# Kernel optimization log

Hardware: AMD Instinct MI355X
Metric: run time of the kernel (lower is better)

Reference implementation:

```python
import jax, jax.numpy as jnp
import numpy as np

B, S, H, E, V = 64, 1024, 1024, 1024, 50257


def setup_inputs() -> dict:
    key = jax.random.key(0)
    ks = jax.random.split(key, 12)
    x = jax.random.randint(ks[0], (B, 1), 0, V, dtype=jnp.int64)
    h = jax.random.normal(ks[1], (B, H), dtype=jnp.float32)
    c = jax.random.normal(ks[2], (B, H), dtype=jnp.float32)
    encoder_output = jax.random.normal(ks[3], (B, S, H), dtype=jnp.float32)
    length = jax.random.randint(ks[4], (B,), 1, S + 1, dtype=jnp.int32)
    length = length.at[0].set(S)  # mask width is length[0]; must equal S
    scale = 0.02
    emb = jax.random.normal(ks[5], (V, E), dtype=jnp.float32) * scale
    W_ih = jax.random.normal(ks[6], (4 * H, E), dtype=jnp.float32) * scale
    b_ih = jnp.zeros((4 * H,), dtype=jnp.float32)
    W_hh = jax.random.normal(ks[7], (4 * H, H), dtype=jnp.float32) * scale
    b_hh = jnp.zeros((4 * H,), dtype=jnp.float32)
    W_bilin = jax.random.normal(ks[8], (H, H), dtype=jnp.float32) * scale
    W_out = jax.random.normal(ks[9], (V, 2 * H), dtype=jnp.float32) * scale
    b_out = jnp.zeros((V,), dtype=jnp.float32)
    return {"x": x, "h": h, "c": c, "encoder_output": encoder_output,
            "length": length, "emb": emb, "W_ih": W_ih, "b_ih": b_ih,
            "W_hh": W_hh, "b_hh": b_hh, "W_bilin": W_bilin,
            "W_out": W_out, "b_out": b_out}


def reference(x, h, c, encoder_output, length, emb, W_ih, b_ih, W_hh, b_hh,
              W_bilin, W_out, b_out):
    # embedding + squeeze(1); dropout is identity in eval mode
    xe = emb[x[:, 0]]  # [B, E]
    # LSTMCell: gates in PyTorch order i, f, g, o
    gates = xe @ W_ih.T + b_ih + h @ W_hh.T + b_hh  # [B, 4H]
    i_g, f_g, g_g, o_g = jnp.split(gates, 4, axis=-1)
    i_g = jax.nn.sigmoid(i_g)
    f_g = jax.nn.sigmoid(f_g)
    g_g = jnp.tanh(g_g)
    o_g = jax.nn.sigmoid(o_g)
    c_new = f_g * c + i_g * g_g
    h_new = o_g * jnp.tanh(c_new)  # [B, H]
    # bilinear attention energy: (h W) . enc
    energy = jnp.einsum('bh,hk,bsk->bs', h_new, W_bilin, encoder_output)
    # mask multiplies energy BEFORE softmax (faithful to original code)
    mask = (jnp.arange(S)[None, :] < length[:, None]).astype(energy.dtype)
    attn = jax.nn.softmax(energy * mask, axis=-1)  # [B, S]
    context = jnp.einsum('bs,bsh->bh', attn, encoder_output)  # [B, H]
    output = jnp.concatenate([context, h_new], axis=1) @ W_out.T + b_out  # [B, V]
    return output, h_new, c_new
```

## Files before the change

kernel.cpp:

```cpp
#include <hip/hip_runtime.h>
#include <math.h>

constexpr int NB = 64;
constexpr int NS = 1024;
constexpr int NH = 1024;
constexpr int NE = 1024;
constexpr int NV = 50257;
constexpr int NK2 = 2048;

typedef __bf16 bf16_8 __attribute__((ext_vector_type(8)));
typedef float  f32x4  __attribute__((ext_vector_type(4)));

__device__ inline f32x4 ntload4(const float* p) {
  return __builtin_nontemporal_load((const f32x4*)p);
}

__global__ __launch_bounds__(256) void k_cvtAg(const int* __restrict__ x,
    const float* __restrict__ h, const float* __restrict__ emb,
    __bf16* __restrict__ Ag) {
  int t = blockIdx.x * 256 + threadIdx.x;
  int b = t >> 11, k = t & 2047;
  float v = (k < NE) ? emb[(size_t)x[b] * NE + k] : h[b * NH + (k - NE)];
  Ag[t] = (__bf16)v;
}

__global__ __launch_bounds__(256) void k_gates_mfma(const __bf16* __restrict__ Ag,
    const float* __restrict__ Wih, const float* __restrict__ bih,
    const float* __restrict__ Whh, const float* __restrict__ bhh,
    float* __restrict__ gates) {
  __shared__ f32x4 red[4][4][64];
  int lane = threadIdx.x & 63;
  int wave = threadIdx.x >> 6;
  int col  = lane & 15;
  int grp  = lane >> 4;
  int j    = blockIdx.x * 16 + col;

  const float* Wsel = (wave < 2) ? Wih : Whh;
  const float*  wp  = Wsel + (size_t)j * 1024 + (wave & 1) * 512 + grp * 8;
  const __bf16* ap  = Ag + wave * 512 + grp * 8;

  f32x4 acc[4] = {};
#pragma unroll 4
  for (int ks = 0; ks < 16; ++ks) {
    int kb = ks * 32;
    f32x4 b0 = ntload4(wp + kb);
    f32x4 b1 = ntload4(wp + kb + 4);
    bf16_8 bf;
    bf[0] = (__bf16)b0[0]; bf[1] = (__bf16)b0[1];
    bf[2] = (__bf16)b0[2]; bf[3] = (__bf16)b0[3];
    bf[4] = (__bf16)b1[0]; bf[5] = (__bf16)b1[1];
    bf[6] = (__bf16)b1[2]; bf[7] = (__bf16)b1[3];
#pragma unroll
    for (int m = 0; m < 4; ++m) {
      bf16_8 a = *(const bf16_8*)(ap + (m * 16 + col) * NK2 + kb);
      acc[m] = __builtin_amdgcn_mfma_f32_16x16x32_bf16(a, bf, acc[m], 0, 0, 0);
    }
  }
#pragma unroll
  for (int m = 0; m < 4; ++m) red[wave][m][lane] = acc[m];
  __syncthreads();
  f32x4 s = red[0][wave][lane];
#pragma unroll
  for (int wv = 1; wv < 4; ++wv) s += red[wv][wave][lane];
  float bias = bih[j] + bhh[j];
  int b = wave * 16 + grp * 4;
#pragma unroll
  for (int r = 0; r < 4; ++r)
    gates[(b + r) * 4096 + j] = s[r] + bias;
}

__global__ __launch_bounds__(256) void k_lstm(const float* __restrict__ gates,
    const float* __restrict__ c, float* __restrict__ hc_out,
    __bf16* __restrict__ A_bf) {
  int t = blockIdx.x * 256 + threadIdx.x;
  int b = t >> 10, hh = t & 1023;
  float ig = gates[b * 4096 + hh];
  float fg = gates[b * 4096 + 1024 + hh];
  float gg = gates[b * 4096 + 2048 + hh];
  float og = gates[b * 4096 + 3072 + hh];
  float i_ = 1.f / (1.f + expf(-ig));
  float f_ = 1.f / (1.f + expf(-fg));
  float g_ = tanhf(gg);
  float o_ = 1.f / (1.f + expf(-og));
  float cn = f_ * c[t] + i_ * g_;
  float hn = o_ * tanhf(cn);
  hc_out[t] = hn;
  hc_out[NB * NH + t] = cn;
  A_bf[b * NK2 + 1024 + hh] = (__bf16)hn;
}

__global__ __launch_bounds__(256) void k_bilin(const float* __restrict__ hnew,
    const float* __restrict__ Wb, float* __restrict__ t_out) {
  int b = blockIdx.x >> 2;
  int k = ((blockIdx.x & 3) << 8) + threadIdx.x;
  const float* hb = hnew + b * NH;
  float acc = 0.f;
#pragma unroll 8
  for (int hh = 0; hh < NH; ++hh)
    acc += hb[hh] * Wb[hh * NH + k];
  t_out[b * NH + k] = acc;
}

__global__ __launch_bounds__(256) void k_attn(const float* __restrict__ t_in,
    const float* __restrict__ enc, const int* __restrict__ length,
    float* __restrict__ ctxp, float* __restrict__ ml) {
  int b     = blockIdx.x >> 4;
  int strip = ((blockIdx.x & 15) << 2) + (threadIdx.x >> 6);
  int lane  = threadIdx.x & 63;
  int len   = length[b];
  int s0    = strip * 16;

  const float* tp = t_in + b * NH;
  f32x4 tv[4];
#pragma unroll
  for (int i = 0; i < 4; ++i) tv[i] = *(const f32x4*)(tp + (i * 64 + lane) * 4);

  const float* ep = enc + ((size_t)b * NS + s0) * NH;

  float m_run = -1e30f, l_run = 0.f;
  f32x4 acc[4] = {};

#pragma unroll 2
  for (int r = 0; r < 16; ++r) {
    f32x4 e[4];
#pragma unroll
    for (int i = 0; i < 4; ++i) e[i] = ntload4(ep + (r * 256 + i * 64 + lane) * 4);
    float d = 0.f;
#pragma unroll
    for (int i = 0; i < 4; ++i)
      d += tv[i][0] * e[i][0] + tv[i][1] * e[i][1] + tv[i][2] * e[i][2] + tv[i][3] * e[i][3];
#pragma unroll
    for (int off = 32; off; off >>= 1) d += __shfl_xor(d, off);
    float v = (s0 + r < len) ? d : 0.f;
    float m_new = fmaxf(m_run, v);
    float f = expf(m_run - m_new);
    float w = expf(v - m_new);
    l_run = l_run * f + w;
#pragma unroll
    for (int i = 0; i < 4; ++i)
      acc[i] = acc[i] * f + w * e[i];
    m_run = m_new;
  }

  int idx = b * 64 + strip;
  float* P = ctxp + (size_t)idx * 1024;
#pragma unroll
  for (int i = 0; i < 4; ++i)
    *(f32x4*)(P + (i * 64 + lane) * 4) = acc[i];
  if (lane == 0) {
    ml[idx * 2]     = m_run;
    ml[idx * 2 + 1] = l_run;
  }
}

__global__ __launch_bounds__(256) void k_attn_combine(const float* __restrict__ ctxp,
    const float* __restrict__ ml, __bf16* __restrict__ A_bf) {
  int b = blockIdx.x;
  int tid = threadIdx.x;
  float M = -1e30f;
#pragma unroll
  for (int c = 0; c < 64; ++c) M = fmaxf(M, ml[(b * 64 + c) * 2]);
  float Z = 0.f;
  f32x4 num = {0.f, 0.f, 0.f, 0.f};
#pragma unroll 4
  for (int c = 0; c < 64; ++c) {
    float e = expf(ml[(b * 64 + c) * 2] - M);
    Z += e * ml[(b * 64 + c) * 2 + 1];
    f32x4 p = *(const f32x4*)(ctxp + ((size_t)(b * 64 + c)) * 1024 + tid * 4);
    num += e * p;
  }
  float inv = 1.f / Z;
  __bf16* dst = A_bf + b * NK2 + tid * 4;
#pragma unroll
  for (int i = 0; i < 4; ++i) dst[i] = (__bf16)(num[i] * inv);
}

__global__ __launch_bounds__(64) void k_out_mfma(const __bf16* __restrict__ A,
    const float* __restrict__ Wout, const float* __restrict__ bout,
    float* __restrict__ out) {
  int lane = threadIdx.x;
  int col  = lane & 15;
  int grp  = lane >> 4;
  int vb   = blockIdx.x * 32;
  int va   = vb + col;
  int vc   = vb + 16 + col;
  int vaC  = va < NV ? va : NV - 1;
  int vcC  = vc < NV ? vc : NV - 1;

  const float*  wpA = Wout + (size_t)vaC * NK2 + grp * 8;
  const float*  wpB = Wout + (size_t)vcC * NK2 + grp * 8;
  const __bf16* ap  = A + grp * 8;

  f32x4 acc[4][2] = {};

#pragma unroll 2
  for (int ks = 0; ks < 64; ++ks) {
    int kb = ks * 32;
    f32x4 a0 = ntload4(wpA + kb);
    f32x4 a1 = ntload4(wpA + kb + 4);
    f32x4 c0 = ntload4(wpB + kb);
    f32x4 c1 = ntload4(wpB + kb + 4);
    bf16_8 bfA, bfB;
    bfA[0] = (__bf16)a0[0]; bfA[1] = (__bf16)a0[1];
    bfA[2] = (__bf16)a0[2]; bfA[3] = (__bf16)a0[3];
    bfA[4] = (__bf16)a1[0]; bfA[5] = (__bf16)a1[1];
    bfA[6] = (__bf16)a1[2]; bfA[7] = (__bf16)a1[3];
    bfB[0] = (__bf16)c0[0]; bfB[1] = (__bf16)c0[1];
    bfB[2] = (__bf16)c0[2]; bfB[3] = (__bf16)c0[3];
    bfB[4] = (__bf16)c1[0]; bfB[5] = (__bf16)c1[1];
    bfB[6] = (__bf16)c1[2]; bfB[7] = (__bf16)c1[3];
#pragma unroll
    for (int m = 0; m < 4; ++m) {
      bf16_8 a = *(const bf16_8*)(ap + (size_t)(m * 16 + col) * NK2 + kb);
      acc[m][0] = __builtin_amdgcn_mfma_f32_16x16x32_bf16(a, bfA, acc[m][0], 0, 0, 0);
      acc[m][1] = __builtin_amdgcn_mfma_f32_16x16x32_bf16(a, bfB, acc[m][1], 0, 0, 0);
    }
  }

#pragma unroll
  for (int n = 0; n < 2; ++n) {
    int vrow = vb + n * 16 + col;
    if (vrow < NV) {
      float bb = bout[vrow];
      int mrow = grp * 4;
#pragma unroll
      for (int m = 0; m < 4; ++m)
#pragma unroll
        for (int r = 0; r < 4; ++r)
          out[(size_t)(m * 16 + mrow + r) * NV + vrow] = acc[m][n][r] + bb;
    }
  }
}

extern "C" void kernel_launch(void* const* d_in, const int* in_sizes, int n_in,
                              void* d_out, int out_size, void* d_ws, size_t ws_size,
                              hipStream_t stream) {
  const int*   x      = (const int*)d_in[0];
  const float* h      = (const float*)d_in[1];
  const float* c      = (const float*)d_in[2];
  const float* enc    = (const float*)d_in[3];
  const int*   length = (const int*)d_in[4];
  const float* emb    = (const float*)d_in[5];
  const float* Wih    = (const float*)d_in[6];
  const float* bih    = (const float*)d_in[7];
  const float* Whh    = (const float*)d_in[8];
  const float* bhh    = (const float*)d_in[9];
  const float* Wb     = (const float*)d_in[10];
  const float* Wout   = (const float*)d_in[11];
  const float* bout   = (const float*)d_in[12];

  float* out = (float*)d_out;
  float* hn  = out + (size_t)NB * NV;

  float* ws      = (float*)d_ws;
  float* gates   = ws;
  float* t_ws    = gates + NB * 4 * NH;
  float* ctxp    = t_ws + NB * NH;
  float* ml      = ctxp + 64 * (size_t)NB * 1024;
  __bf16* A_bf   = (__bf16*)(ml + NB * 128);
  __bf16* Ag_bf  = A_bf + NB * NK2;

  k_cvtAg<<<NB * NK2 / 256, 256, 0, stream>>>(x, h, emb, Ag_bf);
  k_gates_mfma<<<4096 / 16, 256, 0, stream>>>(Ag_bf, Wih, bih, Whh, bhh, gates);
  k_lstm<<<NB * NH / 256, 256, 0, stream>>>(gates, c, hn, A_bf);
  k_bilin<<<NB * 4, 256, 0, stream>>>(hn, Wb, t_ws);
  k_attn<<<NB * 16, 256, 0, stream>>>(t_ws, enc, length, ctxp, ml);
  k_attn_combine<<<NB, 256, 0, stream>>>(ctxp, ml, A_bf);
  k_out_mfma<<<(NV + 31) / 32, 64, 0, stream>>>(A_bf, Wout, bout, out);
}
```

Baseline: 269.7 us.

## Split output GEMM over K and overlap the h-half with attention

The output projection is split into two K halves. The half that multiplies h_new (the upper 1024 columns of W_out) is computed as extra blocks inside the attention kernel, so its W_out streaming runs concurrently with the encoder streaming. The final kernel then handles only the context half and adds the stored partial sums and the bias. The cost is a 64xV fp32 partial buffer that must be written and read back, and the attention kernel now competes with the GEMM blocks for memory bandwidth.

```diff
diff --git a/kernel.cpp b/kernel.cpp
--- a/kernel.cpp
+++ b/kernel.cpp
@@ -101,12 +101,71 @@
   t_out[b * NH + k] = acc;
 }
 
-__global__ __launch_bounds__(256) void k_attn(const float* __restrict__ t_in,
+constexpr int NOUT1 = (NV + 127) / 128;
+
+__global__ __launch_bounds__(256) void k_attn_out1(const float* __restrict__ t_in,
     const float* __restrict__ enc, const int* __restrict__ length,
-    float* __restrict__ ctxp, float* __restrict__ ml) {
-  int b     = blockIdx.x >> 4;
-  int strip = ((blockIdx.x & 15) << 2) + (threadIdx.x >> 6);
-  int lane  = threadIdx.x & 63;
+    const __bf16* __restrict__ A, const float* __restrict__ Wout,
+    float* __restrict__ ctxp, float* __restrict__ ml, float* __restrict__ part) {
+  int tid  = threadIdx.x;
+  int lane = tid & 63;
+
+  if (blockIdx.x < NOUT1) {
+    int wave = tid >> 6;
+    int col  = lane & 15;
+    int grp  = lane >> 4;
+    int vb   = blockIdx.x * 128 + wave * 32;
+    int va   = vb + col;
+    int vc   = vb + 16 + col;
+    int vaC  = va < NV ? va : NV - 1;
+    int vcC  = vc < NV ? vc : NV - 1;
+
+    const float*  wpA = Wout + (size_t)vaC * NK2 + 1024 + grp * 8;
+    const float*  wpB = Wout + (size_t)vcC * NK2 + 1024 + grp * 8;
+    const __bf16* ap  = A + 1024 + grp * 8;
+
+    f32x4 acc[4][2] = {};
+#pragma unroll 2
+    for (int ks = 0; ks < 32; ++ks) {
+      int kb = ks * 32;
+      f32x4 a0 = ntload4(wpA + kb);
+      f32x4 a1 = ntload4(wpA + kb + 4);
+      f32x4 c0 = ntload4(wpB + kb);
+      f32x4 c1 = ntload4(wpB + kb + 4);
+      bf16_8 bfA, bfB;
+      bfA[0] = (__bf16)a0[0]; bfA[1] = (__bf16)a0[1];
+      bfA[2] = (__bf16)a0[2]; bfA[3] = (__bf16)a0[3];
+      bfA[4] = (__bf16)a1[0]; bfA[5] = (__bf16)a1[1];
+      bfA[6] = (__bf16)a1[2]; bfA[7] = (__bf16)a1[3];
+      bfB[0] = (__bf16)c0[0]; bfB[1] = (__bf16)c0[1];
+      bfB[2] = (__bf16)c0[2]; bfB[3] = (__bf16)c0[3];
+      bfB[4] = (__bf16)c1[0]; bfB[5] = (__bf16)c1[1];
+      bfB[6] = (__bf16)c1[2]; bfB[7] = (__bf16)c1[3];
+#pragma unroll
+      for (int m = 0; m < 4; ++m) {
+        bf16_8 a = *(const bf16_8*)(ap + (size_t)(m * 16 + col) * NK2 + kb);
+        acc[m][0] = __builtin_amdgcn_mfma_f32_16x16x32_bf16(a, bfA, acc[m][0], 0, 0, 0);
+        acc[m][1] = __builtin_amdgcn_mfma_f32_16x16x32_bf16(a, bfB, acc[m][1], 0, 0, 0);
+      }
+    }
+#pragma unroll
+    for (int n = 0; n < 2; ++n) {
+      int vrow = vb + n * 16 + col;
+      if (vrow < NV) {
+        int mrow = grp * 4;
+#pragma unroll
+        for (int m = 0; m < 4; ++m)
+#pragma unroll
+          for (int r = 0; r < 4; ++r)
+            part[(size_t)(m * 16 + mrow + r) * NV + vrow] = acc[m][n][r];
+      }
+    }
+    return;
+  }
+
+  int bid   = blockIdx.x - NOUT1;
+  int b     = bid >> 4;
+  int strip = ((bid & 15) << 2) + (tid >> 6);
   int len   = length[b];
   int s0    = strip * 16;
 
@@ -175,9 +234,9 @@
   for (int i = 0; i < 4; ++i) dst[i] = (__bf16)(num[i] * inv);
 }
 
-__global__ __launch_bounds__(64) void k_out_mfma(const __bf16* __restrict__ A,
+__global__ __launch_bounds__(64) void k_out0(const __bf16* __restrict__ A,
     const float* __restrict__ Wout, const float* __restrict__ bout,
-    float* __restrict__ out) {
+    const float* __restrict__ part, float* __restrict__ out) {
   int lane = threadIdx.x;
   int col  = lane & 15;
   int grp  = lane >> 4;
@@ -194,7 +253,7 @@
   f32x4 acc[4][2] = {};
 
 #pragma unroll 2
-  for (int ks = 0; ks < 64; ++ks) {
+  for (int ks = 0; ks < 32; ++ks) {
     int kb = ks * 32;
     f32x4 a0 = ntload4(wpA + kb);
     f32x4 a1 = ntload4(wpA + kb + 4);
@@ -226,8 +285,10 @@
 #pragma unroll
       for (int m = 0; m < 4; ++m)
 #pragma unroll
-        for (int r = 0; r < 4; ++r)
-          out[(size_t)(m * 16 + mrow + r) * NV + vrow] = acc[m][n][r] + bb;
+        for (int r = 0; r < 4; ++r) {
+          size_t o = (size_t)(m * 16 + mrow + r) * NV + vrow;
+          out[o] = acc[m][n][r] + part[o] + bb;
+        }
     }
   }
 }
@@ -259,12 +320,14 @@
   float* ml      = ctxp + 64 * (size_t)NB * 1024;
   __bf16* A_bf   = (__bf16*)(ml + NB * 128);
   __bf16* Ag_bf  = A_bf + NB * NK2;
+  float* poutp   = (float*)(Ag_bf + NB * NK2);
 
   k_cvtAg<<<NB * NK2 / 256, 256, 0, stream>>>(x, h, emb, Ag_bf);
   k_gates_mfma<<<4096 / 16, 256, 0, stream>>>(Ag_bf, Wih, bih, Whh, bhh, gates);
   k_lstm<<<NB * NH / 256, 256, 0, stream>>>(gates, c, hn, A_bf);
   k_bilin<<<NB * 4, 256, 0, stream>>>(hn, Wb, t_ws);
-  k_attn<<<NB * 16, 256, 0, stream>>>(t_ws, enc, length, ctxp, ml);
+  k_attn_out1<<<NOUT1 + NB * 16, 256, 0, stream>>>(t_ws, enc, length, A_bf, Wout,
+                                                   ctxp, ml, poutp);
   k_attn_combine<<<NB, 256, 0, stream>>>(ctxp, ml, A_bf);
-  k_out_mfma<<<(NV + 31) / 32, 64, 0, stream>>>(A_bf, Wout, bout, out);
-}
+  k_out0<<<(NV + 31) / 32, 64, 0, stream>>>(A_bf, Wout, bout, poutp, out);
+}
```

Measured after the change: 279.8 us. 1.04x slower.
